# Performance work log

Measured on AMD Instinct MI355X. Metric: run time of the kernel, lower is better.

Reference implementation:

```python
import jax, jax.numpy as jnp
import numpy as np

NUM_EXPERTS = 64
TOP_K = 8
NORM_TOPK_PROB = True


def setup_inputs() -> dict:
    key = jax.random.key(0)
    k1, k2 = jax.random.split(key)
    hidden_states = jax.random.normal(k1, (8192, 4096), dtype=jnp.float32)
    gate_w = jax.random.normal(k2, (NUM_EXPERTS, 4096), dtype=jnp.float32) * (1.0 / np.sqrt(4096))
    return {"hidden_states": hidden_states, "gate_w": gate_w}


def reference(hidden_states, gate_w):
    # router_logits: (T, E) = hidden @ gate_w.T
    router_logits = jnp.einsum('th,eh->te', hidden_states, gate_w)
    # softmax in float32 (matches F.softmax(..., dtype=torch.float32))
    router_probs = jax.nn.softmax(router_logits.astype(jnp.float32), axis=-1)
    # top-k selection (descending, like torch.topk)
    expert_weights, expert_indices = jax.lax.top_k(router_probs, TOP_K)
    if NORM_TOPK_PROB:
        expert_weights = expert_weights / jnp.sum(expert_weights, axis=-1, keepdims=True)
    expert_weights = expert_weights.astype(hidden_states.dtype)
    # load-balancing loss: N_e * sum_i f_i * p_i
    num_tokens = router_probs.shape[0]
    one_hot = jax.nn.one_hot(expert_indices, NUM_EXPERTS, dtype=jnp.float32)  # (T, K, E)
    tokens_per_expert = one_hot.sum(axis=(0, 1))                              # (E,)
    f = tokens_per_expert / (num_tokens * TOP_K)
    p = router_probs.mean(axis=0)
    aux_loss = NUM_EXPERTS * jnp.sum(f * p)
    return (expert_weights, expert_indices, aux_loss)
```

## Files before the change

kernel.cpp:

```cpp
#include <hip/hip_runtime.h>
#include <math.h>

#define HDIM 4096
#define NEXP 64
#define NTOK 8192
#define KSPLIT 16
#define KSLICE (HDIM / KSPLIT)
#define BM 128
#define CHUNK 32
#define NCHUNK (KSLICE / CHUNK)
#define AUXCOPIES 32
#define AUXF (AUXCOPIES * 128)
#define TPW 2
#define TOPK_BLOCKS (NTOK / (4 * TPW))

typedef short short8 __attribute__((ext_vector_type(8)));
typedef float f32x4 __attribute__((ext_vector_type(4)));
typedef const __attribute__((address_space(1))) unsigned int* gas_t;
typedef __attribute__((address_space(3))) unsigned int* las_t;

__device__ __forceinline__ void split2x3(float x0, float x1, int& h, int& md, int& lo) {
  unsigned u0 = __float_as_uint(x0), u1 = __float_as_uint(x1);
  unsigned h0 = u0 & 0xFFFF0000u, h1 = u1 & 0xFFFF0000u;
  float r0 = x0 - __uint_as_float(h0);
  float r1 = x1 - __uint_as_float(h1);
  unsigned m0 = __float_as_uint(r0) & 0xFFFF0000u;
  unsigned m1 = __float_as_uint(r1) & 0xFFFF0000u;
  float s0 = r0 - __uint_as_float(m0);
  float s1 = r1 - __uint_as_float(m1);
  h  = (int)((h0 >> 16) | h1);
  md = (int)((m0 >> 16) | m1);
  lo = (int)((__float_as_uint(s0) >> 16) | (__float_as_uint(s1) & 0xFFFF0000u));
}

__device__ __forceinline__ short8 pack_s8(int a, int b, int c, int d) {
  union { int i[4]; short8 s; } u;
  u.i[0] = a; u.i[1] = b; u.i[2] = c; u.i[3] = d;
  return u.s;
}

__global__ __launch_bounds__(256, 4) void gemm_k(const float* __restrict__ A,
                                                 const float* __restrict__ W,
                                                 float* __restrict__ Lp,
                                                 float* __restrict__ auxbuf,
                                                 int atomic_mode) {
  __shared__ __align__(16) float As[2][BM * CHUNK];
  const int tid = threadIdx.x;
  if (blockIdx.x == 0 && blockIdx.y == 0) {
#pragma unroll
    for (int t = tid; t < AUXF; t += 256) auxbuf[t] = 0.f;
  }
  const int m_base = blockIdx.x * BM;
  const int k_base = blockIdx.y * KSLICE;
  float* Lout = Lp + (atomic_mode ? (size_t)0 : (size_t)blockIdx.y * NTOK * NEXP);

  const int lane = tid & 63;
  const int wave = tid >> 6;
  const int l15 = lane & 15;
  const int quad = lane >> 4;
  const int wm = wave * 32;

  const int rowp = wave * 32 + (lane >> 3);
  const int cblk = (lane & 7) ^ (lane >> 3);
  const float* gA0 = A + (size_t)(m_base + rowp) * HDIM + k_base + cblk * 4;

  auto stageA = [&](int i, int buf) {
#pragma unroll
    for (int j = 0; j < 4; ++j) {
      const float* src = gA0 + (size_t)(j * 8) * HDIM + i * CHUNK;
      __builtin_amdgcn_global_load_lds((gas_t)(const void*)src,
                                       (las_t)(void*)&As[buf][(wave * 4 + j) * 256],
                                       16, 0, 0);
    }
  };

  const float* gW = W + (size_t)l15 * HDIM + k_base + quad * 8;

  f32x4 acc[2][4];
#pragma unroll
  for (int mt = 0; mt < 2; ++mt)
#pragma unroll
    for (int nt = 0; nt < 4; ++nt) acc[mt][nt] = (f32x4){0.f, 0.f, 0.f, 0.f};

  stageA(0, 0);

  for (int i = 0; i < NCHUNK; ++i) {
    const int buf = i & 1;
    asm volatile("s_waitcnt vmcnt(0)" ::: "memory");
    __builtin_amdgcn_sched_barrier(0);

    float4 bw[4][2];
#pragma unroll
    for (int nt = 0; nt < 4; ++nt) {
      const float* wp = gW + (size_t)(nt * 16) * HDIM + i * CHUNK;
      bw[nt][0] = *(const float4*)wp;
      bw[nt][1] = *(const float4*)(wp + 4);
    }
    float4 a0[2], a1[2];
#pragma unroll
    for (int mt = 0; mt < 2; ++mt) {
      const int r = wm + mt * 16 + l15;
      const int rb = r * CHUNK;
      const int sw = r & 7;
      a0[mt] = *(const float4*)&As[buf][rb + ((2 * quad) ^ sw) * 4];
      a1[mt] = *(const float4*)&As[buf][rb + ((2 * quad + 1) ^ sw) * 4];
    }
    __builtin_amdgcn_sched_barrier(0);

    if (i + 1 < NCHUNK) stageA(i + 1, buf ^ 1);
    __builtin_amdgcn_sched_barrier(0);

    short8 fa[2][3];
#pragma unroll
    for (int mt = 0; mt < 2; ++mt) {
      const float f[8] = {a0[mt].x, a0[mt].y, a0[mt].z, a0[mt].w,
                          a1[mt].x, a1[mt].y, a1[mt].z, a1[mt].w};
      int h[4], md[4], lo[4];
#pragma unroll
      for (int j = 0; j < 4; ++j) split2x3(f[2 * j], f[2 * j + 1], h[j], md[j], lo[j]);
      fa[mt][0] = pack_s8(h[0], h[1], h[2], h[3]);
      fa[mt][1] = pack_s8(md[0], md[1], md[2], md[3]);
      fa[mt][2] = pack_s8(lo[0], lo[1], lo[2], lo[3]);
    }

#pragma unroll
    for (int nt = 0; nt < 4; ++nt) {
      const float fb[8] = {bw[nt][0].x, bw[nt][0].y, bw[nt][0].z, bw[nt][0].w,
                           bw[nt][1].x, bw[nt][1].y, bw[nt][1].z, bw[nt][1].w};
      int h[4], md[4], lo[4];
#pragma unroll
      for (int j = 0; j < 4; ++j) split2x3(fb[2 * j], fb[2 * j + 1], h[j], md[j], lo[j]);
      const short8 bh = pack_s8(h[0], h[1], h[2], h[3]);
      const short8 bmid = pack_s8(md[0], md[1], md[2], md[3]);
      const short8 blo = pack_s8(lo[0], lo[1], lo[2], lo[3]);
#pragma unroll
      for (int mt = 0; mt < 2; ++mt) {
        f32x4 c = acc[mt][nt];
        c = __builtin_amdgcn_mfma_f32_16x16x32_bf16(fa[mt][0], bh, c, 0, 0, 0);
        c = __builtin_amdgcn_mfma_f32_16x16x32_bf16(fa[mt][0], bmid, c, 0, 0, 0);
        c = __builtin_amdgcn_mfma_f32_16x16x32_bf16(fa[mt][1], bh, c, 0, 0, 0);
        c = __builtin_amdgcn_mfma_f32_16x16x32_bf16(fa[mt][0], blo, c, 0, 0, 0);
        c = __builtin_amdgcn_mfma_f32_16x16x32_bf16(fa[mt][2], bh, c, 0, 0, 0);
        c = __builtin_amdgcn_mfma_f32_16x16x32_bf16(fa[mt][1], bmid, c, 0, 0, 0);
        acc[mt][nt] = c;
      }
    }
  }

#pragma unroll
  for (int mt = 0; mt < 2; ++mt)
#pragma unroll
    for (int nt = 0; nt < 4; ++nt)
#pragma unroll
      for (int r = 0; r < 4; ++r) {
        const int m = m_base + wm + mt * 16 + quad * 4 + r;
        const int n = nt * 16 + l15;
        if (atomic_mode) atomicAdd(&Lout[(size_t)m * NEXP + n], acc[mt][nt][r]);
        else Lout[(size_t)m * NEXP + n] = acc[mt][nt][r];
      }
}

__global__ __launch_bounds__(256) void topk_k(const float* __restrict__ Lp, int nsl,
                                              float* __restrict__ out,
                                              float* __restrict__ auxbuf) {
  __shared__ float sl[2][4][64];
  __shared__ float s_aux[128];
  const int tid = threadIdx.x;
  const int wave = tid >> 6, lane = tid & 63;
  if (tid < 128) s_aux[tid] = 0.f;

  const int t0 = (blockIdx.x * 4 + wave) * TPW;
  float x0 = 0.f, x1 = 0.f;
  if (nsl == KSPLIT) {
    float v[2][KSPLIT];
#pragma unroll
    for (int tok = 0; tok < 2; ++tok)
#pragma unroll
      for (int s = 0; s < KSPLIT; ++s)
        v[tok][s] = Lp[(size_t)s * (NTOK * NEXP) + (size_t)(t0 + tok) * NEXP + lane];
#pragma unroll
    for (int s = 0; s < KSPLIT; ++s) { x0 += v[0][s]; x1 += v[1][s]; }
  } else {
    for (int s = 0; s < nsl; ++s) {
      x0 += Lp[(size_t)s * (NTOK * NEXP) + (size_t)t0 * NEXP + lane];
      x1 += Lp[(size_t)s * (NTOK * NEXP) + (size_t)(t0 + 1) * NEXP + lane];
    }
  }
  sl[0][wave][lane] = x0;
  sl[1][wave][lane] = x1;

  float m0 = x0, m1 = x1;
#pragma unroll
  for (int off = 32; off >= 1; off >>= 1) {
    m0 = fmaxf(m0, __shfl_xor(m0, off, 64));
    m1 = fmaxf(m1, __shfl_xor(m1, off, 64));
  }
  const float e0 = __expf(x0 - m0), e1 = __expf(x1 - m1);
  float ss0 = e0, ss1 = e1;
#pragma unroll
  for (int off = 32; off >= 1; off >>= 1) {
    ss0 += __shfl_xor(ss0, off, 64);
    ss1 += __shfl_xor(ss1, off, 64);
  }
  const float p0 = e0 / ss0, p1 = e1 / ss1;

  __syncthreads();

  int c0 = 0, c1 = 0;
#pragma unroll
  for (int c = 0; c < 4; ++c) {
#pragma unroll
    for (int tok = 0; tok < 2; ++tok) {
      const float4 w0 = *(const float4*)&sl[tok][wave][c * 16 + 0];
      const float4 w1 = *(const float4*)&sl[tok][wave][c * 16 + 4];
      const float4 w2 = *(const float4*)&sl[tok][wave][c * 16 + 8];
      const float4 w3 = *(const float4*)&sl[tok][wave][c * 16 + 12];
      const float xv[16] = {w0.x, w0.y, w0.z, w0.w, w1.x, w1.y, w1.z, w1.w,
                            w2.x, w2.y, w2.z, w2.w, w3.x, w3.y, w3.z, w3.w};
      const float xr = tok ? x1 : x0;
      int cc = 0;
#pragma unroll
      for (int j = 0; j < 16; ++j) {
        const int jj = c * 16 + j;
        cc += (xv[j] > xr) || (xv[j] == xr && jj < lane);
      }
      if (tok) c1 += cc; else c0 += cc;
    }
  }

  float tp0 = (c0 < 8) ? p0 : 0.f;
  float tp1 = (c1 < 8) ? p1 : 0.f;
  float ts0 = tp0, ts1 = tp1;
#pragma unroll
  for (int off = 32; off >= 1; off >>= 1) {
    ts0 += __shfl_xor(ts0, off, 64);
    ts1 += __shfl_xor(ts1, off, 64);
  }

  const float pv0 = __uint_as_float(
      (unsigned)__builtin_amdgcn_ds_permute(c0 << 2, (int)__float_as_uint(p0)));
  const int pi0 = __builtin_amdgcn_ds_permute(c0 << 2, lane);
  const float pv1 = __uint_as_float(
      (unsigned)__builtin_amdgcn_ds_permute(c1 << 2, (int)__float_as_uint(p1)));
  const int pi1 = __builtin_amdgcn_ds_permute(c1 << 2, lane);
  if (lane < 8) {
    out[(size_t)t0 * 8 + lane] = pv0 / ts0;
    out[(size_t)NTOK * 8 + (size_t)t0 * 8 + lane] = (float)pi0;
    out[(size_t)(t0 + 1) * 8 + lane] = pv1 / ts1;
    out[(size_t)NTOK * 8 + (size_t)(t0 + 1) * 8 + lane] = (float)pi1;
  }
  atomicAdd(&s_aux[lane], p0 + p1);
  const float cadd = (c0 < 8 ? 1.f : 0.f) + (c1 < 8 ? 1.f : 0.f);
  atomicAdd(&s_aux[64 + lane], cadd);

  __syncthreads();
  if (tid < 128)
    atomicAdd(&auxbuf[(blockIdx.x & (AUXCOPIES - 1)) * 128 + tid], s_aux[tid]);
}

__global__ void aux_k(const float* __restrict__ auxbuf, float* __restrict__ out) {
  const int e = threadIdx.x;
  float p = 0.f, f = 0.f;
#pragma unroll
  for (int c = 0; c < AUXCOPIES; ++c) {
    p += auxbuf[c * 128 + e];
    f += auxbuf[c * 128 + 64 + e];
  }
  p *= (1.f / (float)NTOK);
  f *= (1.f / ((float)NTOK * 8.f));
  float v = f * p;
#pragma unroll
  for (int off = 32; off >= 1; off >>= 1) v += __shfl_xor(v, off, 64);
  if (e == 0) out[2 * NTOK * 8] = 64.f * v;
}

extern "C" void kernel_launch(void* const* d_in, const int* in_sizes, int n_in,
                              void* d_out, int out_size, void* d_ws, size_t ws_size,
                              hipStream_t stream) {
  const float* hidden = (const float*)d_in[0];
  const float* gate = (const float*)d_in[1];
  float* out = (float*)d_out;
  float* ws = (float*)d_ws;
  float* auxbuf = ws;
  float* slices = ws + AUXF;

  const size_t need = (size_t)AUXF * 4 + (size_t)KSPLIT * NTOK * NEXP * 4;
  const int atomic_mode = (ws_size < need) ? 1 : 0;
  const int nsl = atomic_mode ? 1 : KSPLIT;

  if (atomic_mode)
    hipMemsetAsync(d_ws, 0, (size_t)AUXF * 4 + (size_t)NTOK * NEXP * 4, stream);

  gemm_k<<<dim3(64, KSPLIT), 256, 0, stream>>>(hidden, gate, slices, auxbuf,
                                               atomic_mode);
  topk_k<<<TOPK_BLOCKS, 256, 0, stream>>>(slices, nsl, out, auxbuf);
  aux_k<<<1, 64, 0, stream>>>(auxbuf, out);
}
```

Before: 225.6 us.

## Load A tiles directly into registers instead of staging through LDS

Replaces the LDS double-buffer fed by global_load_lds with direct per-lane float4 loads of A into a register double buffer, prefetching the next chunk while converting the current one. Partial vmcnt waits let the W conversion and MFMAs start before the A prefetch lands. This removes LDS traffic and its swizzle reads, at the cost of higher register pressure, so launch bounds drop from 4 to 3 waves per SIMD. Each lane now reads a strided 32-byte row slice straight from global memory, which may coalesce worse than the previous staged layout.

```diff
diff --git a/kernel.cpp b/kernel.cpp
--- a/kernel.cpp
+++ b/kernel.cpp
@@ -16,8 +16,6 @@
 
 typedef short short8 __attribute__((ext_vector_type(8)));
 typedef float f32x4 __attribute__((ext_vector_type(4)));
-typedef const __attribute__((address_space(1))) unsigned int* gas_t;
-typedef __attribute__((address_space(3))) unsigned int* las_t;
 
 __device__ __forceinline__ void split2x3(float x0, float x1, int& h, int& md, int& lo) {
   unsigned u0 = __float_as_uint(x0), u1 = __float_as_uint(x1);
@@ -39,12 +37,11 @@
   return u.s;
 }
 
-__global__ __launch_bounds__(256, 4) void gemm_k(const float* __restrict__ A,
+__global__ __launch_bounds__(256, 3) void gemm_k(const float* __restrict__ A,
                                                  const float* __restrict__ W,
                                                  float* __restrict__ Lp,
                                                  float* __restrict__ auxbuf,
                                                  int atomic_mode) {
-  __shared__ __align__(16) float As[2][BM * CHUNK];
   const int tid = threadIdx.x;
   if (blockIdx.x == 0 && blockIdx.y == 0) {
 #pragma unroll
@@ -60,20 +57,10 @@
   const int quad = lane >> 4;
   const int wm = wave * 32;
 
-  const int rowp = wave * 32 + (lane >> 3);
-  const int cblk = (lane & 7) ^ (lane >> 3);
-  const float* gA0 = A + (size_t)(m_base + rowp) * HDIM + k_base + cblk * 4;
-
-  auto stageA = [&](int i, int buf) {
-#pragma unroll
-    for (int j = 0; j < 4; ++j) {
-      const float* src = gA0 + (size_t)(j * 8) * HDIM + i * CHUNK;
-      __builtin_amdgcn_global_load_lds((gas_t)(const void*)src,
-                                       (las_t)(void*)&As[buf][(wave * 4 + j) * 256],
-                                       16, 0, 0);
-    }
-  };
-
+  const float* gA[2];
+#pragma unroll
+  for (int mt = 0; mt < 2; ++mt)
+    gA[mt] = A + (size_t)(m_base + wm + mt * 16 + l15) * HDIM + k_base + quad * 8;
   const float* gW = W + (size_t)l15 * HDIM + k_base + quad * 8;
 
   f32x4 acc[2][4];
@@ -82,39 +69,44 @@
 #pragma unroll
     for (int nt = 0; nt < 4; ++nt) acc[mt][nt] = (f32x4){0.f, 0.f, 0.f, 0.f};
 
-  stageA(0, 0);
-
+  float4 aA[2][2][2];
+
+#pragma unroll
+  for (int mt = 0; mt < 2; ++mt) {
+    aA[0][mt][0] = *(const float4*)(gA[mt]);
+    aA[0][mt][1] = *(const float4*)(gA[mt] + 4);
+  }
+
+#pragma unroll
   for (int i = 0; i < NCHUNK; ++i) {
-    const int buf = i & 1;
+    const int ph = i & 1;
     asm volatile("s_waitcnt vmcnt(0)" ::: "memory");
     __builtin_amdgcn_sched_barrier(0);
 
-    float4 bw[4][2];
+    float4 w[4][2];
 #pragma unroll
     for (int nt = 0; nt < 4; ++nt) {
       const float* wp = gW + (size_t)(nt * 16) * HDIM + i * CHUNK;
-      bw[nt][0] = *(const float4*)wp;
-      bw[nt][1] = *(const float4*)(wp + 4);
-    }
-    float4 a0[2], a1[2];
+      w[nt][0] = *(const float4*)wp;
+      w[nt][1] = *(const float4*)(wp + 4);
+    }
+    __builtin_amdgcn_sched_barrier(0);
+
+    if (i + 1 < NCHUNK) {
+#pragma unroll
+      for (int mt = 0; mt < 2; ++mt) {
+        aA[ph ^ 1][mt][0] = *(const float4*)(gA[mt] + (i + 1) * CHUNK);
+        aA[ph ^ 1][mt][1] = *(const float4*)(gA[mt] + (i + 1) * CHUNK + 4);
+      }
+    }
+    __builtin_amdgcn_sched_barrier(0);
+
+    short8 fa[2][3];
 #pragma unroll
     for (int mt = 0; mt < 2; ++mt) {
-      const int r = wm + mt * 16 + l15;
-      const int rb = r * CHUNK;
-      const int sw = r & 7;
-      a0[mt] = *(const float4*)&As[buf][rb + ((2 * quad) ^ sw) * 4];
-      a1[mt] = *(const float4*)&As[buf][rb + ((2 * quad + 1) ^ sw) * 4];
-    }
-    __builtin_amdgcn_sched_barrier(0);
-
-    if (i + 1 < NCHUNK) stageA(i + 1, buf ^ 1);
-    __builtin_amdgcn_sched_barrier(0);
-
-    short8 fa[2][3];
-#pragma unroll
-    for (int mt = 0; mt < 2; ++mt) {
-      const float f[8] = {a0[mt].x, a0[mt].y, a0[mt].z, a0[mt].w,
-                          a1[mt].x, a1[mt].y, a1[mt].z, a1[mt].w};
+      const float f[8] = {aA[ph][mt][0].x, aA[ph][mt][0].y, aA[ph][mt][0].z,
+                          aA[ph][mt][0].w, aA[ph][mt][1].x, aA[ph][mt][1].y,
+                          aA[ph][mt][1].z, aA[ph][mt][1].w};
       int h[4], md[4], lo[4];
 #pragma unroll
       for (int j = 0; j < 4; ++j) split2x3(f[2 * j], f[2 * j + 1], h[j], md[j], lo[j]);
@@ -123,10 +115,14 @@
       fa[mt][2] = pack_s8(lo[0], lo[1], lo[2], lo[3]);
     }
 
+    if (i + 1 < NCHUNK) asm volatile("s_waitcnt vmcnt(4)" ::: "memory");
+    else                asm volatile("s_waitcnt vmcnt(0)" ::: "memory");
+    __builtin_amdgcn_sched_barrier(0);
+
 #pragma unroll
     for (int nt = 0; nt < 4; ++nt) {
-      const float fb[8] = {bw[nt][0].x, bw[nt][0].y, bw[nt][0].z, bw[nt][0].w,
-                           bw[nt][1].x, bw[nt][1].y, bw[nt][1].z, bw[nt][1].w};
+      const float fb[8] = {w[nt][0].x, w[nt][0].y, w[nt][0].z, w[nt][0].w,
+                           w[nt][1].x, w[nt][1].y, w[nt][1].z, w[nt][1].w};
       int h[4], md[4], lo[4];
 #pragma unroll
       for (int j = 0; j < 4; ++j) split2x3(fb[2 * j], fb[2 * j + 1], h[j], md[j], lo[j]);
```

Result: slower. 243.4 us (+7.9%).
